# Kernel tuning notes

Hardware: AMD Instinct MI355X
Metric: run time of the kernel (lower is better)

Reference implementation:

```python
import jax, jax.numpy as jnp
import numpy as np

T, B, D = 2048, 2, 768
N, HD = 12, 64  # num_heads, head_dim; N*HD == D


def _rel_shift(s):
    # s: [I, J, B, N] -> Transformer-XL relative shift along J
    I, J, b, n = s.shape
    s = jnp.pad(s, ((0, 0), (1, 0), (0, 0), (0, 0)))  # [I, J+1, B, N]
    s = s.reshape(J + 1, I, b, n)[1:]                  # drop first row after transpose-view
    return s.reshape(I, J, b, n)


def setup_inputs() -> dict:
    key = jax.random.key(0)
    ks = jax.random.split(key, 8)
    x = jax.random.normal(ks[0], (T, B, D), dtype=jnp.float32)
    pos_encodings = jax.random.normal(ks[1], (T, D), dtype=jnp.float32)
    u_bias = jax.random.normal(ks[2], (N, HD), dtype=jnp.float32) * 0.02
    v_bias = jax.random.normal(ks[3], (N, HD), dtype=jnp.float32) * 0.02
    # causal mask: True = masked (j > i)
    attn_mask = jnp.triu(jnp.ones((T, T), dtype=bool), k=1)
    W_qkv = jax.random.normal(ks[4], (D, 3 * N * HD), dtype=jnp.float32) * 0.02
    W_pos = jax.random.normal(ks[5], (D, N * HD), dtype=jnp.float32) * 0.02
    W_out = jax.random.normal(ks[6], (N * HD, D), dtype=jnp.float32) * 0.02
    return {"x": x, "pos_encodings": pos_encodings, "u_bias": u_bias,
            "v_bias": v_bias, "W_qkv": W_qkv, "W_pos": W_pos,
            "W_out": W_out, "attn_mask": attn_mask}


def reference(x, pos_encodings, u_bias, v_bias, W_qkv, W_pos, W_out, attn_mask):
    tgt, bsz, dim = x.shape
    n, hd = u_bias.shape
    scale = 1.0 / (dim ** 0.5)  # NOTE: original scales by 1/sqrt(dim), not head_dim

    qkv = x @ W_qkv                                   # [T, B, 3*N*HD]
    q, k, v = jnp.split(qkv, 3, axis=-1)
    q = q.reshape(tgt, bsz, n, hd)
    k = k.reshape(tgt, bsz, n, hd)
    v = v.reshape(tgt, bsz, n, hd)
    pos = (pos_encodings @ W_pos).reshape(-1, n, hd)  # [P, N, HD]

    content_score = jnp.einsum('ibnd,jbnd->ijbn', q + u_bias, k)
    pos_score = jnp.einsum('ibnd,jnd->ijbn', q + v_bias, pos)
    pos_score = _rel_shift(pos_score)

    attn_score = (content_score + pos_score) * scale  # [T, S, B, N]
    attn_score = jnp.where(attn_mask[:, :, None, None], -jnp.inf, attn_score)
    attn = jax.nn.softmax(attn_score, axis=1)

    context = jnp.einsum('ijbn,jbnd->ibnd', attn, v)
    context = context.reshape(tgt, bsz, n * hd)
    return context @ W_out                            # [T, B, D]
```

## Files before the change

### kernel.cpp

```cpp
#include <hip/hip_runtime.h>
#include <math.h>

#define T_SEQ 2048
#define BSZ   2
#define DIM   768
#define NH    12
#define SCALE_L2 0.05205877f

typedef float f32x4 __attribute__((ext_vector_type(4)));
typedef __bf16 bf16x8 __attribute__((ext_vector_type(8)));
typedef unsigned int uint_t;
typedef unsigned short us16;

static __device__ __forceinline__ f32x4 mfma16(bf16x8 a, bf16x8 b, f32x4 c) {
    return __builtin_amdgcn_mfma_f32_16x16x32_bf16(a, b, c, 0, 0, 0);
}
static __device__ __forceinline__ us16 f2bf(float f) {
    uint_t u = __builtin_bit_cast(uint_t, f);
    u += 0x7fff + ((u >> 16) & 1);
    return (us16)(u >> 16);
}
static __device__ __forceinline__ us16 f2bf_up(float f) {
    return (us16)((__builtin_bit_cast(uint_t, f) + 0x8000u) >> 16);
}
static __device__ __forceinline__ float bf2f(us16 h) {
    return __builtin_bit_cast(float, (uint_t)h << 16);
}
static __device__ __forceinline__ bf16x8 ld_frag(const us16* p) {
    union { uint4 u; bf16x8 b; } x;
    x.u = *(const uint4*)p;
    return x.b;
}

typedef __attribute__((address_space(1))) const unsigned int guint;
typedef __attribute__((address_space(3))) unsigned int luint;
static __device__ __forceinline__ void glds16(const us16* g, us16* l) {
    __builtin_amdgcn_global_load_lds((guint*)g, (luint*)l, 16, 0, 0);
}

__constant__ int SLOT_IB[40] = {15,15,15,15, 14,14,14,14, 13,13,13,13, 12,12,12,12,
                                11,11,11, 10,10,10, 9,9,9, 8,8,8,
                                7,7, 6,6, 5,5, 4,4, 3, 2, 1, 0};
__constant__ int SLOT_C0[40] = {0,8,16,24, 0,8,16,24, 0,8,16,24, 0,8,16,24,
                                0,8,16, 0,8,16, 0,8,16, 0,8,16,
                                0,8, 0,8, 0,8, 0,8, 0, 0, 0, 0};
__constant__ int SLOT_C1[40] = {8,16,24,32, 8,16,24,30, 8,16,24,28, 8,16,24,26,
                                8,16,24, 8,16,22, 8,16,20, 8,16,18,
                                8,16, 8,14, 8,12, 8,10, 8, 6, 4, 2};
__constant__ int CB_BASE[12] = {34,32,30,28, 25,22,19,16, 12,8,4,0};
__constant__ int CB_N[12]    = {2,2,2,2, 3,3,3,3, 4,4,4,4};

__global__ __launch_bounds__(256)
void cvt_bf16_2(const float* __restrict__ in0, us16* __restrict__ out0, int n0,
                const float* __restrict__ in1, us16* __restrict__ out1, int n1) {
    int idx = blockIdx.x * 256 + threadIdx.x;
    int stride = gridDim.x * 256;
    int ntot = n0 + n1;
    for (int i = idx; i < ntot; i += stride) {
        const float4* src;
        ushort4* dst;
        if (i < n0) { src = (const float4*)in0 + i; dst = (ushort4*)out0 + i; }
        else        { src = (const float4*)in1 + (i - n0); dst = (ushort4*)out1 + (i - n0); }
        float4 f = *src;
        ushort4 o;
        o.x = f2bf(f.x); o.y = f2bf(f.y); o.z = f2bf(f.z); o.w = f2bf(f.w);
        *dst = o;
    }
}

__global__ __launch_bounds__(256)
void cvt_t3(const float* __restrict__ w0, us16* __restrict__ o0,
            const float* __restrict__ w1, us16* __restrict__ o1,
            const float* __restrict__ w2, us16* __restrict__ o2) {
    __shared__ us16 Ts[64][72];
    const int bid = blockIdx.x;
    const float* in; us16* out; int C, bx, by;
    if (bid < 432)      { in = w0; out = o0; C = 2304; bx = bid % 36;        by = bid / 36; }
    else if (bid < 576) { in = w1; out = o1; C = 768;  bx = (bid - 432) % 12; by = (bid - 432) / 12; }
    else                { in = w2; out = o2; C = 768;  bx = (bid - 576) % 12; by = (bid - 576) / 12; }
    const int R = 768;
    const int tid = threadIdx.x;
    const int c0 = bx * 64, r0 = by * 64;
    {
        const int r = tid >> 2, cq = (tid & 3) * 16;
        const float* src = in + (size_t)(r0 + r) * C + c0 + cq;
        #pragma unroll
        for (int i = 0; i < 4; ++i) {
            float4 f = *(const float4*)(src + i * 4);
            Ts[cq + i * 4 + 0][r] = f2bf(f.x);
            Ts[cq + i * 4 + 1][r] = f2bf(f.y);
            Ts[cq + i * 4 + 2][r] = f2bf(f.z);
            Ts[cq + i * 4 + 3][r] = f2bf(f.w);
        }
    }
    __syncthreads();
    {
        const int oc = tid >> 2, rq = (tid & 3) * 16;
        us16* dst = out + (size_t)(c0 + oc) * R + r0 + rq;
        *(uint4*)dst       = *(uint4*)&Ts[oc][rq];
        *(uint4*)(dst + 8) = *(uint4*)&Ts[oc][rq + 8];
    }
}

template <typename OutT>
static __device__ __forceinline__
void gemm_body(const us16* __restrict__ A, const us16* __restrict__ Bt,
               OutT* __restrict__ C, int N, int K, int m0, int n0,
               us16* As , us16* Bs ) {
    const int tid  = threadIdx.x;
    const int lane = tid & 63;
    const int w    = tid >> 6;
    const int g    = lane >> 4;
    const int lm   = lane & 15;
    const int wm = (w >> 1) * 64, wn = (w & 1) * 64;

    const int nc0 = (w * 2 + 0) * 64 + lane;
    const int nc1 = (w * 2 + 1) * 64 + lane;
    const us16* as0 = A  + (size_t)(m0 + (nc0 >> 2)) * K + (nc0 & 3) * 8;
    const us16* as1 = A  + (size_t)(m0 + (nc1 >> 2)) * K + (nc1 & 3) * 8;
    const us16* bs0 = Bt + (size_t)(n0 + (nc0 >> 2)) * K + (nc0 & 3) * 8;
    const us16* bs1 = Bt + (size_t)(n0 + (nc1 >> 2)) * K + (nc1 & 3) * 8;

    f32x4 acc[4][4];
    #pragma unroll
    for (int i = 0; i < 4; ++i)
        #pragma unroll
        for (int j = 0; j < 4; ++j) acc[i][j] = (f32x4){0.f, 0.f, 0.f, 0.f};

    auto STAGE = [&](int buf) {
        glds16(as0, &As[buf * 4096 + (w * 2 + 0) * 512]);
        glds16(as1, &As[buf * 4096 + (w * 2 + 1) * 512]);
        glds16(bs0, &Bs[buf * 4096 + (w * 2 + 0) * 512]);
        glds16(bs1, &Bs[buf * 4096 + (w * 2 + 1) * 512]);
        as0 += 32; as1 += 32; bs0 += 32; bs1 += 32;
    };
    auto COMPUTE = [&](int buf) {
        bf16x8 af[4], bfr[4];
        #pragma unroll
        for (int mi = 0; mi < 4; ++mi)
            af[mi]  = ld_frag(&As[buf * 4096 + (wm + mi * 16 + lm) * 32 + g * 8]);
        #pragma unroll
        for (int ni = 0; ni < 4; ++ni)
            bfr[ni] = ld_frag(&Bs[buf * 4096 + (wn + ni * 16 + lm) * 32 + g * 8]);
        #pragma unroll
        for (int mi = 0; mi < 4; ++mi)
            #pragma unroll
            for (int ni = 0; ni < 4; ++ni)
                acc[mi][ni] = mfma16(af[mi], bfr[ni], acc[mi][ni]);
    };

    const int nsteps = K / 32;
    STAGE(0);
    __syncthreads();
    for (int it = 0; it < nsteps / 2; ++it) {
        STAGE(1);
        COMPUTE(0);
        __syncthreads();
        if (it * 2 + 2 < nsteps) STAGE(0);
        COMPUTE(1);
        __syncthreads();
    }

    #pragma unroll
    for (int mi = 0; mi < 4; ++mi) {
        #pragma unroll
        for (int reg = 0; reg < 4; ++reg) {
            int row = m0 + wm + mi * 16 + g * 4 + reg;
            OutT* crow = C + (size_t)row * N + n0 + wn + lm;
            #pragma unroll
            for (int ni = 0; ni < 4; ++ni) {
                float v = acc[mi][ni][reg];
                if constexpr (sizeof(OutT) == 2)
                    *(us16*)&crow[ni * 16] = f2bf(v);
                else
                    crow[ni * 16] = v;
            }
        }
    }
}

__global__ __launch_bounds__(256)
void gemm_dual(const us16* __restrict__ A0, const us16* __restrict__ B0, us16* __restrict__ C0,
               const us16* __restrict__ A1, const us16* __restrict__ B1, us16* __restrict__ C1) {
    __shared__ us16 As[2 * 128 * 32];
    __shared__ us16 Bs[2 * 128 * 32];
    const int bid = blockIdx.x;
    if (bid < 576) {
        gemm_body<us16>(A0, B0, C0, 2304, 768, (bid / 18) * 128, (bid % 18) * 128, As, Bs);
    } else {
        const int b = bid - 576;
        gemm_body<us16>(A1, B1, C1, 768, 768, (b / 6) * 128, (b % 6) * 128, As, Bs);
    }
}

__global__ __launch_bounds__(256)
void gemm_out(const us16* __restrict__ A, const us16* __restrict__ Bt,
              float* __restrict__ C) {
    __shared__ us16 As[2 * 128 * 32];
    __shared__ us16 Bs[2 * 128 * 32];
    gemm_body<float>(A, Bt, C, 768, 768, (int)blockIdx.y * 128, (int)blockIdx.x * 128, As, Bs);
}

__global__ __launch_bounds__(512, 4)
void attn_mfma(const us16* __restrict__ qkvb, const us16* __restrict__ posb,
               const float* __restrict__ u_bias, const float* __restrict__ v_bias,
               us16* __restrict__ ctx, float* __restrict__ pO, float* __restrict__ pML)
{
    __shared__ us16 Ks[64][72];
    __shared__ us16 Vt[80][72];
    __shared__ us16 Band[256][72];
    __shared__ us16 Ps[8][16][72];

    const int tid  = threadIdx.x;
    const int lane = tid & 63;
    const int w    = tid >> 6;
    const int g    = lane >> 4;
    const int lm   = lane & 15;

    const int flat = (int)blockIdx.y * 40 + (int)blockIdx.x;
    const int wid  = (flat & 7) * 120 + (flat >> 3);
    const int slot = wid % 40;
    const int y    = wid / 40;

    const int ib = SLOT_IB[slot];
    const int c0 = SLOT_C0[slot], c1 = SLOT_C1[slot];
    const int i0 = ib * 128;
    const int n  = y % NH, b = y / NH;
    const int i_w0 = i0 + w * 16;
    const bool multi = (ib >= 4);

    for (int idx = tid; idx < 576; idx += 512) {
        int r = idx / 36, c = (idx % 36) * 2;
        *(uint_t*)&Vt[64 + r][c] = 0x3F803F80u;
    }

    bf16x8 Qu[2], Qv[2];
    {
        const int qi = i_w0 + lm;
        const us16* qrow = qkvb + (size_t)(qi * BSZ + b) * 2304 + n * 64;
        #pragma unroll
        for (int ks = 0; ks < 2; ++ks) {
            const int h0 = ks * 32 + g * 8;
            union { uint4 u; us16 s[8]; } q;
            q.u = *(const uint4*)(qrow + h0);
            union { bf16x8 bv; us16 s[8]; } fu, fv;
            #pragma unroll
            for (int e = 0; e < 8; ++e) {
                float f  = bf2f(q.s[e]);
                fu.s[e] = f2bf((f + u_bias[n * 64 + h0 + e]) * SCALE_L2);
                fv.s[e] = f2bf((f + v_bias[n * 64 + h0 + e]) * SCALE_L2);
            }
            Qu[ks] = fu.bv; Qv[ks] = fv.bv;
        }
    }

    const int jr = tid >> 3, cc = (tid & 7) * 8;
    const int jp = tid & 31, hb = (tid >> 5) * 4;
    {
        const int j0 = c0 * 64;
        *(uint4*)&Ks[jr][cc] =
            *(const uint4*)(qkvb + (size_t)((j0 + jr) * BSZ + b) * 2304 + 768 + n * 64 + cc);
        const us16* v0 = qkvb + (size_t)((j0 + 2 * jp) * BSZ + b) * 2304 + 1536 + n * 64 + hb;
        union { uint2 u; us16 s[4]; } r0, r1;
        r0.u = *(const uint2*)v0;
        r1.u = *(const uint2*)(v0 + 2 * 2304);
        #pragma unroll
        for (int k = 0; k < 4; ++k)
            *(uint_t*)&Vt[hb + k][2 * jp] = (uint_t)r0.s[k] | ((uint_t)r1.s[k] << 16);
        const int t_min0 = T_SEQ - 128 - i0 + j0;
        #pragma unroll
        for (int pass = 0; pass < 3; ++pass) {
            int t = t_min0 + pass * 64 + jr;
            uint4 val = make_uint4(0u, 0u, 0u, 0u);
            if (t < T_SEQ)
                val = *(const uint4*)(posb + (size_t)t * DIM + n * 64 + cc);
            *(uint4*)&Band[t & 255][cc] = val;
        }
    }
    __syncthreads();

    f32x4 Oacc[5];
    #pragma unroll
    for (int hs = 0; hs < 5; ++hs) Oacc[hs] = (f32x4){0.f, 0.f, 0.f, 0.f};
    float m = -INFINITY;

    const int base_w = 112 - 16 * w;

    uint4 sK, sB;
    uint2 sV0, sV1;

    for (int jt = c0; jt < c1; ++jt) {
        const int j0 = jt * 64;
        const int t_min = T_SEQ - 128 - i0 + j0;
        const bool pf = (jt + 1 < c1);

        if (pf) {
            const int j0n = j0 + 64;
            sK = *(const uint4*)(qkvb + (size_t)((j0n + jr) * BSZ + b) * 2304 + 768 + n * 64 + cc);
            const us16* v0 = qkvb + (size_t)((j0n + 2 * jp) * BSZ + b) * 2304 + 1536 + n * 64 + hb;
            sV0 = *(const uint2*)v0;
            sV1 = *(const uint2*)(v0 + 2 * 2304);
            const int t_new = t_min + 192 + jr;
            sB = make_uint4(0u, 0u, 0u, 0u);
            if (t_new < T_SEQ)
                sB = *(const uint4*)(posb + (size_t)t_new * DIM + n * 64 + cc);
        }

        __builtin_amdgcn_s_setprio(1);
        f32x4 R[5];
        {
            const int rb = t_min + base_w + lm;
            #pragma unroll
            for (int gs = 0; gs < 5; ++gs) {
                const int row = (rb + gs * 16) & 255;
                f32x4 a = (f32x4){0.f, 0.f, 0.f, 0.f};
                a = mfma16(Qv[0], ld_frag(&Band[row][g * 8]), a);
                a = mfma16(Qv[1], ld_frag(&Band[row][32 + g * 8]), a);
                R[gs] = a;
            }
        }
        f32x4 S4[4];
        #pragma unroll
        for (int js = 0; js < 4; ++js) {
            f32x4 s4 = (f32x4){0.f, 0.f, 0.f, 0.f};
            s4 = mfma16(Qu[0], ld_frag(&Ks[js * 16 + lm][g * 8]), s4);
            s4 = mfma16(Qu[1], ld_frag(&Ks[js * 16 + lm][32 + g * 8]), s4);
            S4[js] = s4;
        }
        __builtin_amdgcn_s_setprio(0);

        float sv[4][4];
        if (j0 + 63 <= i_w0) {
            #pragma unroll
            for (int reg = 0; reg < 4; ++reg) {
                const int r   = g * 4 + reg;
                const int idx = lm + 15 - r;
                const int rot = (lane & 48) | (idx & 15);
                #pragma unroll
                for (int js = 0; js < 4; ++js) {
                    float va = __shfl(R[js][reg], rot);
                    float vb = __shfl(R[js + 1][reg], rot);
                    sv[js][reg] = S4[js][reg] + ((idx & 16) ? vb : va);
                }
            }
        } else {
            #pragma unroll
            for (int reg = 0; reg < 4; ++reg) {
                const int r   = g * 4 + reg;
                const int idx = lm + 15 - r;
                const int rot = (lane & 48) | (idx & 15);
                #pragma unroll
                for (int js = 0; js < 4; ++js) {
                    float va = __shfl(R[js][reg], rot);
                    float vb = __shfl(R[js + 1][reg], rot);
                    float rv = (idx & 16) ? vb : va;
                    int jg = j0 + js * 16 + lm;
                    sv[js][reg] = (jg <= i_w0 + r) ? (S4[js][reg] + rv) : -INFINITY;
                }
            }
        }

        float tm = sv[0][0];
        #pragma unroll
        for (int js = 0; js < 4; ++js)
            #pragma unroll
            for (int reg = 0; reg < 4; ++reg) tm = fmaxf(tm, sv[js][reg]);
        #pragma unroll
        for (int d = 1; d < 16; d <<= 1) tm = fmaxf(tm, __shfl_xor(tm, d));
        if (tm > m + 8.0f) {
            float alpha = __builtin_amdgcn_exp2f(m - tm);
            m = tm;
            #pragma unroll
            for (int hs = 0; hs < 5; ++hs)
                #pragma unroll
                for (int reg = 0; reg < 4; ++reg) Oacc[hs][reg] *= alpha;
        }

        #pragma unroll
        for (int reg = 0; reg < 4; ++reg) {
            const int r = g * 4 + reg;
            #pragma unroll
            for (int js = 0; js < 4; ++js) {
                float p = __builtin_amdgcn_exp2f(sv[js][reg] - m);
                Ps[w][r][js * 16 + lm] = f2bf_up(p);
            }
        }

        __builtin_amdgcn_s_setprio(1);
        #pragma unroll
        for (int ks = 0; ks < 2; ++ks) {
            bf16x8 Pf = ld_frag(&Ps[w][lm][ks * 32 + g * 8]);
            #pragma unroll
            for (int hs = 0; hs < 5; ++hs) {
                bf16x8 Vf = ld_frag(&Vt[hs * 16 + lm][ks * 32 + g * 8]);
                Oacc[hs] = mfma16(Pf, Vf, Oacc[hs]);
            }
        }
        __builtin_amdgcn_s_setprio(0);

        if (pf) {
            __syncthreads();
            *(uint4*)&Ks[jr][cc] = sK;
            union { uint2 u; us16 s[4]; } r0, r1;
            r0.u = sV0; r1.u = sV1;
            #pragma unroll
            for (int k = 0; k < 4; ++k)
                *(uint_t*)&Vt[hb + k][2 * jp] = (uint_t)r0.s[k] | ((uint_t)r1.s[k] << 16);
            const int t_new = t_min + 192 + jr;
            *(uint4*)&Band[t_new & 255][cc] = sB;
            __syncthreads();
        }
    }

    if (multi) {
        const size_t pbase = ((size_t)y * 36 + slot) * 128;
        #pragma unroll
        for (int reg = 0; reg < 4; ++reg) {
            const int r = w * 16 + g * 4 + reg;
            float* orow = pO + (pbase + r) * 64 + lm;
            #pragma unroll
            for (int hs = 0; hs < 4; ++hs) orow[hs * 16] = Oacc[hs][reg];
            if (lm == 0) {
                pML[(pbase + r) * 2 + 0] = m;
                pML[(pbase + r) * 2 + 1] = Oacc[4][reg];
            }
        }
    } else {
        #pragma unroll
        for (int reg = 0; reg < 4; ++reg) {
            const int ig = i_w0 + g * 4 + reg;
            float inv = 1.0f / Oacc[4][reg];
            us16* crow = ctx + (size_t)(ig * BSZ + b) * DIM + n * 64;
            #pragma unroll
            for (int hs = 0; hs < 4; ++hs)
                crow[hs * 16 + lm] = f2bf(Oacc[hs][reg] * inv);
        }
    }
}

__global__ __launch_bounds__(256)
void attn_combine(const float* __restrict__ pO, const float* __restrict__ pML,
                  us16* __restrict__ ctx) {
    const int ib = 4 + blockIdx.x;
    const int y  = blockIdx.y;
    const int n = y % NH, b = y / NH;
    const int base = CB_BASE[blockIdx.x], nc = CB_N[blockIdx.x];
    const int tid = threadIdx.x;
    const int r = tid >> 1, half = (tid & 1) * 32;

    float mc[4], lc[4], sc[4];
    float mstar = -INFINITY;
    #pragma unroll
    for (int c = 0; c < 4; ++c) {
        mc[c] = -INFINITY; lc[c] = 0.f;
        if (c < nc) {
            const float* ml = pML + ((size_t)(y * 36 + base + c) * 128 + r) * 2;
            mc[c] = ml[0]; lc[c] = ml[1];
        }
        mstar = fmaxf(mstar, mc[c]);
    }
    float lstar = 0.f;
    #pragma unroll
    for (int c = 0; c < 4; ++c) {
        sc[c] = (c < nc) ? __builtin_amdgcn_exp2f(mc[c] - mstar) : 0.f;
        lstar += sc[c] * lc[c];
    }
    const float inv = 1.0f / lstar;

    f32x4 acc[8];
    #pragma unroll
    for (int k = 0; k < 8; ++k) acc[k] = (f32x4){0.f, 0.f, 0.f, 0.f};
    #pragma unroll
    for (int c = 0; c < 4; ++c) {
        if (c < nc) {
            const f32x4* src = (const f32x4*)(pO + ((size_t)(y * 36 + base + c) * 128 + r) * 64 + half);
            float s = sc[c];
            #pragma unroll
            for (int k = 0; k < 8; ++k) acc[k] += src[k] * s;
        }
    }
    const int ig = ib * 128 + r;
    us16* crow = ctx + (size_t)(ig * BSZ + b) * DIM + n * 64 + half;
    #pragma unroll
    for (int k = 0; k < 8; ++k) {
        us16 q[4];
        #pragma unroll
        for (int e = 0; e < 4; ++e) q[e] = f2bf(acc[k][e] * inv);
        *(uint2*)&crow[k * 4] = *(uint2*)q;
    }
}

extern "C" void kernel_launch(void* const* d_in, const int* in_sizes, int n_in,
                              void* d_out, int out_size, void* d_ws, size_t ws_size,
                              hipStream_t stream) {
    const float* x      = (const float*)d_in[0];
    const float* pe     = (const float*)d_in[1];
    const float* u_bias = (const float*)d_in[2];
    const float* v_bias = (const float*)d_in[3];
    const float* W_qkv  = (const float*)d_in[4];
    const float* W_pos  = (const float*)d_in[5];
    const float* W_out  = (const float*)d_in[6];
    float* out = (float*)d_out;

    char* ws = (char*)d_ws;
    us16*  qkvb  = (us16*)(ws);
    us16*  posb  = (us16*)(ws + 18874368);
    us16*  ctxb  = (us16*)(ws + 22020096);
    us16*  Woutb = (us16*)(ws + 28311552);
    float* pML   = (float*)(ws + 29491200);
    float* pO    = (float*)(ws + 30375936);
    us16*  xb    = (us16*)(ws + 30375936);
    us16*  peb   = (us16*)(ws + 36667392);
    us16*  Wqkvb = (us16*)(ws + 39813120);
    us16*  Wposb = (us16*)(ws + 43352064);

    dim3 blk(256);
    cvt_bf16_2<<<1024, blk, 0, stream>>>(x, xb, 4096 * 768 / 4, pe, peb, 2048 * 768 / 4);
    cvt_t3<<<720, blk, 0, stream>>>(W_qkv, Wqkvb, W_pos, Wposb, W_out, Woutb);
    gemm_dual<<<672, blk, 0, stream>>>(xb, Wqkvb, qkvb, peb, Wposb, posb);
    attn_mfma<<<dim3(40, 24), dim3(512), 0, stream>>>(qkvb, posb, u_bias, v_bias, ctxb, pO, pML);
    attn_combine<<<dim3(12, 24), blk, 0, stream>>>(pO, pML, ctxb);
    gemm_out<<<dim3(768 / 128, 4096 / 128), blk, 0, stream>>>(ctxb, Woutb, out);
}
```

Before: 145.3 us.

## Fuse fp32-to-bf16 activation conversion into projection GEMM A-operand staging

Drops the separate conversion kernel for x and pos_encodings. The dual projection GEMM now loads fp32 A tiles into registers, converts them with a hardware bf16 cast and writes them to LDS, while B tiles keep the async global-to-LDS path. This removes one kernel launch and the round trip of writing and re-reading bf16 activation copies. In exchange the GEMM reads twice as many A bytes per tile, holds extra registers, and the register-staged path may overlap less well than the async LDS loads.

```diff
diff --git a/kernel.cpp b/kernel.cpp
--- a/kernel.cpp
+++ b/kernel.cpp
@@ -19,6 +19,10 @@
     uint_t u = __builtin_bit_cast(uint_t, f);
     u += 0x7fff + ((u >> 16) & 1);
     return (us16)(u >> 16);
+}
+static __device__ __forceinline__ us16 f2bf_hw(float f) {
+    __bf16 h = (__bf16)f;
+    return __builtin_bit_cast(us16, h);
 }
 static __device__ __forceinline__ us16 f2bf_up(float f) {
     return (us16)((__builtin_bit_cast(uint_t, f) + 0x8000u) >> 16);
@@ -49,24 +53,6 @@
                                 8,16, 8,14, 8,12, 8,10, 8, 6, 4, 2};
 __constant__ int CB_BASE[12] = {34,32,30,28, 25,22,19,16, 12,8,4,0};
 __constant__ int CB_N[12]    = {2,2,2,2, 3,3,3,3, 4,4,4,4};
-
-__global__ __launch_bounds__(256)
-void cvt_bf16_2(const float* __restrict__ in0, us16* __restrict__ out0, int n0,
-                const float* __restrict__ in1, us16* __restrict__ out1, int n1) {
-    int idx = blockIdx.x * 256 + threadIdx.x;
-    int stride = gridDim.x * 256;
-    int ntot = n0 + n1;
-    for (int i = idx; i < ntot; i += stride) {
-        const float4* src;
-        ushort4* dst;
-        if (i < n0) { src = (const float4*)in0 + i; dst = (ushort4*)out0 + i; }
-        else        { src = (const float4*)in1 + (i - n0); dst = (ushort4*)out1 + (i - n0); }
-        float4 f = *src;
-        ushort4 o;
-        o.x = f2bf(f.x); o.y = f2bf(f.y); o.z = f2bf(f.z); o.w = f2bf(f.w);
-        *dst = o;
-    }
-}
 
 __global__ __launch_bounds__(256)
 void cvt_t3(const float* __restrict__ w0, us16* __restrict__ o0,
@@ -102,9 +88,9 @@
     }
 }
 
-template <typename OutT>
+template <bool F32A, typename AT, typename OutT>
 static __device__ __forceinline__
-void gemm_body(const us16* __restrict__ A, const us16* __restrict__ Bt,
+void gemm_body(const AT* __restrict__ A, const us16* __restrict__ Bt,
                OutT* __restrict__ C, int N, int K, int m0, int n0,
                us16* As , us16* Bs ) {
     const int tid  = threadIdx.x;
@@ -116,23 +102,57 @@
 
     const int nc0 = (w * 2 + 0) * 64 + lane;
     const int nc1 = (w * 2 + 1) * 64 + lane;
-    const us16* as0 = A  + (size_t)(m0 + (nc0 >> 2)) * K + (nc0 & 3) * 8;
-    const us16* as1 = A  + (size_t)(m0 + (nc1 >> 2)) * K + (nc1 & 3) * 8;
     const us16* bs0 = Bt + (size_t)(n0 + (nc0 >> 2)) * K + (nc0 & 3) * 8;
     const us16* bs1 = Bt + (size_t)(n0 + (nc1 >> 2)) * K + (nc1 & 3) * 8;
 
+    const us16* as0 = nullptr;
+    const us16* as1 = nullptr;
+    const float* afp = nullptr;
+    const int ar = tid >> 1, ac = (tid & 1) * 16;
+    if constexpr (F32A) {
+        afp = (const float*)A + (size_t)(m0 + ar) * K + ac;
+    } else {
+        as0 = (const us16*)A + (size_t)(m0 + (nc0 >> 2)) * K + (nc0 & 3) * 8;
+        as1 = (const us16*)A + (size_t)(m0 + (nc1 >> 2)) * K + (nc1 & 3) * 8;
+    }
+
     f32x4 acc[4][4];
     #pragma unroll
     for (int i = 0; i < 4; ++i)
         #pragma unroll
         for (int j = 0; j < 4; ++j) acc[i][j] = (f32x4){0.f, 0.f, 0.f, 0.f};
 
-    auto STAGE = [&](int buf) {
+    float4 ra0, ra1, ra2, ra3;
+
+    auto STAGE_B = [&](int buf) {
+        glds16(bs0, &Bs[buf * 4096 + (w * 2 + 0) * 512]);
+        glds16(bs1, &Bs[buf * 4096 + (w * 2 + 1) * 512]);
+        bs0 += 32; bs1 += 32;
+    };
+    auto STAGE_A_G = [&](int buf) {
         glds16(as0, &As[buf * 4096 + (w * 2 + 0) * 512]);
         glds16(as1, &As[buf * 4096 + (w * 2 + 1) * 512]);
-        glds16(bs0, &Bs[buf * 4096 + (w * 2 + 0) * 512]);
-        glds16(bs1, &Bs[buf * 4096 + (w * 2 + 1) * 512]);
-        as0 += 32; as1 += 32; bs0 += 32; bs1 += 32;
+        as0 += 32; as1 += 32;
+    };
+    auto A_LOAD = [&]() {
+        ra0 = *(const float4*)(afp + 0);
+        ra1 = *(const float4*)(afp + 4);
+        ra2 = *(const float4*)(afp + 8);
+        ra3 = *(const float4*)(afp + 12);
+        afp += 32;
+    };
+    auto A_WRITE = [&](int buf) {
+        union { uint4 v[2]; us16 s[16]; } t;
+        t.s[0]  = f2bf_hw(ra0.x); t.s[1]  = f2bf_hw(ra0.y);
+        t.s[2]  = f2bf_hw(ra0.z); t.s[3]  = f2bf_hw(ra0.w);
+        t.s[4]  = f2bf_hw(ra1.x); t.s[5]  = f2bf_hw(ra1.y);
+        t.s[6]  = f2bf_hw(ra1.z); t.s[7]  = f2bf_hw(ra1.w);
+        t.s[8]  = f2bf_hw(ra2.x); t.s[9]  = f2bf_hw(ra2.y);
+        t.s[10] = f2bf_hw(ra2.z); t.s[11] = f2bf_hw(ra2.w);
+        t.s[12] = f2bf_hw(ra3.x); t.s[13] = f2bf_hw(ra3.y);
+        t.s[14] = f2bf_hw(ra3.z); t.s[15] = f2bf_hw(ra3.w);
+        *(uint4*)&As[buf * 4096 + ar * 32 + ac]     = t.v[0];
+        *(uint4*)&As[buf * 4096 + ar * 32 + ac + 8] = t.v[1];
     };
     auto COMPUTE = [&](int buf) {
         bf16x8 af[4], bfr[4];
@@ -150,14 +170,25 @@
     };
 
     const int nsteps = K / 32;
-    STAGE(0);
+    if constexpr (F32A) A_LOAD();
+    STAGE_B(0);
+    if constexpr (F32A) A_WRITE(0); else STAGE_A_G(0);
     __syncthreads();
     for (int it = 0; it < nsteps / 2; ++it) {
-        STAGE(1);
+        const bool more = (it * 2 + 2 < nsteps);
+        if constexpr (F32A) A_LOAD();
+        STAGE_B(1);
+        if constexpr (!F32A) STAGE_A_G(1);
         COMPUTE(0);
+        if constexpr (F32A) A_WRITE(1);
         __syncthreads();
-        if (it * 2 + 2 < nsteps) STAGE(0);
+        if (more) {
+            if constexpr (F32A) A_LOAD();
+            STAGE_B(0);
+            if constexpr (!F32A) STAGE_A_G(0);
+        }
         COMPUTE(1);
+        if (more) { if constexpr (F32A) A_WRITE(0); }
         __syncthreads();
     }
 
@@ -180,16 +211,16 @@
 }
 
 __global__ __launch_bounds__(256)
-void gemm_dual(const us16* __restrict__ A0, const us16* __restrict__ B0, us16* __restrict__ C0,
-               const us16* __restrict__ A1, const us16* __restrict__ B1, us16* __restrict__ C1) {
+void gemm_dual(const float* __restrict__ A0, const us16* __restrict__ B0, us16* __restrict__ C0,
+               const float* __restrict__ A1, const us16* __restrict__ B1, us16* __restrict__ C1) {
     __shared__ us16 As[2 * 128 * 32];
     __shared__ us16 Bs[2 * 128 * 32];
     const int bid = blockIdx.x;
     if (bid < 576) {
-        gemm_body<us16>(A0, B0, C0, 2304, 768, (bid / 18) * 128, (bid % 18) * 128, As, Bs);
+        gemm_body<true, float, us16>(A0, B0, C0, 2304, 768, (bid / 18) * 128, (bid % 18) * 128, As, Bs);
     } else {
         const int b = bid - 576;
-        gemm_body<us16>(A1, B1, C1, 768, 768, (b / 6) * 128, (b % 6) * 128, As, Bs);
+        gemm_body<true, float, us16>(A1, B1, C1, 768, 768, (b / 6) * 128, (b % 6) * 128, As, Bs);
     }
 }
 
@@ -198,7 +229,7 @@
               float* __restrict__ C) {
     __shared__ us16 As[2 * 128 * 32];
     __shared__ us16 Bs[2 * 128 * 32];
-    gemm_body<float>(A, Bt, C, 768, 768, (int)blockIdx.y * 128, (int)blockIdx.x * 128, As, Bs);
+    gemm_body<false, us16, float>(A, Bt, C, 768, 768, (int)blockIdx.y * 128, (int)blockIdx.x * 128, As, Bs);
 }
 
 __global__ __launch_bounds__(512, 4)
@@ -509,15 +540,12 @@
     us16*  Woutb = (us16*)(ws + 28311552);
     float* pML   = (float*)(ws + 29491200);
     float* pO    = (float*)(ws + 30375936);
-    us16*  xb    = (us16*)(ws + 30375936);
-    us16*  peb   = (us16*)(ws + 36667392);
-    us16*  Wqkvb = (us16*)(ws + 39813120);
-    us16*  Wposb = (us16*)(ws + 43352064);
+    us16*  Wqkvb = (us16*)(ws + 30375936);
+    us16*  Wposb = (us16*)(ws + 33914880);
 
     dim3 blk(256);
-    cvt_bf16_2<<<1024, blk, 0, stream>>>(x, xb, 4096 * 768 / 4, pe, peb, 2048 * 768 / 4);
     cvt_t3<<<720, blk, 0, stream>>>(W_qkv, Wqkvb, W_pos, Wposb, W_out, Woutb);
-    gemm_dual<<<672, blk, 0, stream>>>(xb, Wqkvb, qkvb, peb, Wposb, posb);
+    gemm_dual<<<672, blk, 0, stream>>>(x, Wqkvb, qkvb, pe, Wposb, posb);
     attn_mfma<<<dim3(40, 24), dim3(512), 0, stream>>>(qkvb, posb, u_bias, v_bias, ctxb, pO, pML);
     attn_combine<<<dim3(12, 24), blk, 0, stream>>>(pO, pML, ctxb);
     gemm_out<<<dim3(768 / 128, 4096 / 128), blk, 0, stream>>>(ctxb, Woutb, out);
```

Result: slower. 168.9 us (+16.3%).
